# Kernel tuning notes

Hardware: AMD Instinct MI355X
Metric: run time of the kernel (lower is better)

## Reference

```python
import jax, jax.numpy as jnp
import numpy as np

D_MODEL = 1024
HIDDEN = 2048            # hidden_dimension // num_smaller_experts_per_expert
E_ROUTED = 14            # total_num_experts*num_smaller - num_shared
E_SHARED = 2
TOP_K = 2                # num_activated*num_smaller - num_shared
EPS = 1e-9               # config.epsilon
RMS_EPS = 1.1920929e-07  # torch RMSNorm default eps=None -> finfo(float32).eps


def setup_inputs() -> dict:
    key = jax.random.key(0)
    ks = jax.random.split(key, 9)
    B, T = 2, 1024
    x = jax.random.normal(ks[0], (B, T, D_MODEL), dtype=jnp.float32)
    router_w = jax.random.normal(ks[1], (D_MODEL, E_ROUTED), dtype=jnp.float32) * 0.006
    rms_w = jnp.ones((E_ROUTED, D_MODEL), dtype=jnp.float32)
    w1 = jax.random.normal(ks[2], (E_ROUTED, D_MODEL, HIDDEN), dtype=jnp.float32) * 0.02
    w2 = jax.random.normal(ks[3], (E_ROUTED, HIDDEN, D_MODEL), dtype=jnp.float32) * 0.02
    rms_w_s = jnp.ones((E_SHARED, D_MODEL), dtype=jnp.float32)
    w1_s = jax.random.normal(ks[4], (E_SHARED, D_MODEL, HIDDEN), dtype=jnp.float32) * 0.02
    w2_s = jax.random.normal(ks[5], (E_SHARED, HIDDEN, D_MODEL), dtype=jnp.float32) * 0.02
    return {"x": x, "router_w": router_w, "rms_w": rms_w, "w1": w1, "w2": w2,
            "rms_w_s": rms_w_s, "w1_s": w1_s, "w2_s": w2_s}


def _ffn(xn, rw, W1, W2):
    # RMSNorm -> Linear -> SiLU -> Linear (dropout is identity in eval)
    ms = jnp.mean(xn * xn, axis=-1, keepdims=True)
    h = (xn * jax.lax.rsqrt(ms + RMS_EPS)) * rw
    return jax.nn.silu(h @ W1) @ W2


def reference(x, router_w, rms_w, w1, w2, rms_w_s, w1_s, w2_s):
    B, T, D = x.shape
    N = B * T
    xf = x.reshape(N, D)
    # router gates + top-k sparsification + renormalization
    gates = jax.nn.softmax(xf @ router_w, axis=-1)          # [N, E]
    top_v, top_i = jax.lax.top_k(gates, TOP_K)              # [N, K]
    masked = jnp.zeros_like(gates).at[jnp.arange(N)[:, None], top_i].set(top_v)
    masked = masked / (masked.sum(axis=-1, keepdims=True) + EPS)  # [N, E]
    # routed experts: compute each expert on all tokens, combine with sparse gate weights
    # (same math as dispatch/index_add combine since masked is 0 off the top-k)
    routed = jax.vmap(lambda rw_, W1_, W2_: _ffn(xf, rw_, W1_, W2_))(rms_w, w1, w2)  # [E, N, D]
    routed_out = jnp.einsum('end,ne->nd', routed, masked)
    # shared experts: unweighted sum
    shared = jax.vmap(lambda rw_, W1_, W2_: _ffn(xf, rw_, W1_, W2_))(rms_w_s, w1_s, w2_s).sum(0)
    return (routed_out + shared).reshape(B, T, D)
```

## Files before the change

### kernel.cpp

```cpp
#include <hip/hip_runtime.h>
#include <hip/hip_bf16.h>
#include <cstdint>
#include <cstddef>

#define D_MODEL 1024
#define HIDDEN 2048
#define E_ROUTED 14
#define E_TOT 16
#define NTOK 2048
#define NASSIGN 4096
#define NROWS 8192

typedef __bf16 bf16x8 __attribute__((ext_vector_type(8)));
typedef float f32x4 __attribute__((ext_vector_type(4)));

static __device__ __forceinline__ unsigned short f2b(float f) {
  unsigned int u = __builtin_bit_cast(unsigned int, f);
  u += 0x7fffu + ((u >> 16) & 1u);
  return (unsigned short)(u >> 16);
}

#define ASYNC_COPY16(gptr, lptr)                                                        \
  __builtin_amdgcn_global_load_lds(                                                     \
      (const __attribute__((address_space(1))) unsigned int*)(gptr),                    \
      (__attribute__((address_space(3))) unsigned int*)(lptr), 16, 0, 0)

__global__ __launch_bounds__(256) void router_kernel(
    const float* __restrict__ x, const float* __restrict__ rweight,
    int* __restrict__ topi, float* __restrict__ topw,
    unsigned short* __restrict__ xhat) {
  int n = blockIdx.x, tid = threadIdx.x;
  const float4 xv = reinterpret_cast<const float4*>(x + (size_t)n * D_MODEL)[tid];
  float ss = xv.x * xv.x + xv.y * xv.y + xv.z * xv.z + xv.w * xv.w;
  float lg[E_ROUTED];
#pragma unroll
  for (int e = 0; e < E_ROUTED; ++e) lg[e] = 0.f;
  const float xa[4] = {xv.x, xv.y, xv.z, xv.w};
#pragma unroll
  for (int i = 0; i < 4; ++i) {
    const float* rw = rweight + (size_t)(tid * 4 + i) * E_ROUTED;
    float xd = xa[i];
#pragma unroll
    for (int e = 0; e < E_ROUTED; ++e) lg[e] = fmaf(xd, rw[e], lg[e]);
  }
#pragma unroll
  for (int off = 32; off > 0; off >>= 1) {
    ss += __shfl_xor(ss, off);
#pragma unroll
    for (int e = 0; e < E_ROUTED; ++e) lg[e] += __shfl_xor(lg[e], off);
  }
  __shared__ float red[4][16];
  int wid = tid >> 6, lane = tid & 63;
  if (lane == 0) {
    red[wid][0] = ss;
#pragma unroll
    for (int e = 0; e < E_ROUTED; ++e) red[wid][1 + e] = lg[e];
  }
  __syncthreads();
  __shared__ float s_scale;
  if (tid == 0) {
    float fin[15];
    for (int v = 0; v < 15; ++v) fin[v] = red[0][v] + red[1][v] + red[2][v] + red[3][v];
    s_scale = rsqrtf(fin[0] * (1.f / D_MODEL) + 1.1920929e-07f);
    float mx = fin[1];
    for (int e = 1; e < E_ROUTED; ++e) mx = fmaxf(mx, fin[1 + e]);
    float p[E_ROUTED]; float Z = 0.f;
    for (int e = 0; e < E_ROUTED; ++e) { p[e] = __expf(fin[1 + e] - mx); Z += p[e]; }
    int i0 = 0; float v0 = p[0];
    for (int e = 1; e < E_ROUTED; ++e) if (p[e] > v0) { v0 = p[e]; i0 = e; }
    int i1 = (i0 == 0) ? 1 : 0; float v1 = p[i1];
    for (int e = 0; e < E_ROUTED; ++e) if (e != i0 && p[e] > v1) { v1 = p[e]; i1 = e; }
    v0 /= Z; v1 /= Z;
    float inv = 1.f / (v0 + v1 + 1e-9f);
    topi[2 * n] = i0; topi[2 * n + 1] = i1;
    topw[2 * n] = v0 * inv; topw[2 * n + 1] = v1 * inv;
  }
  __syncthreads();
  float sc = s_scale;
  ushort4 hx;
  hx.x = f2b(xv.x * sc); hx.y = f2b(xv.y * sc);
  hx.z = f2b(xv.z * sc); hx.w = f2b(xv.w * sc);
  reinterpret_cast<ushort4*>(xhat + (size_t)n * D_MODEL)[tid] = hx;
}

__global__ __launch_bounds__(256) void count_kernel(const int* __restrict__ topi,
                                                    int* __restrict__ goff,
                                                    int* __restrict__ cursor) {
  __shared__ int cnt[E_ROUTED];
  int tid = threadIdx.x;
  if (tid < E_ROUTED) cnt[tid] = 0;
  __syncthreads();
  for (int i = tid; i < NASSIGN; i += 256) atomicAdd(&cnt[topi[i]], 1);
  __syncthreads();
  if (tid == 0) {
    int acc = 0;
    for (int e = 0; e < E_ROUTED; ++e) { goff[e] = acc; cursor[e] = acc; acc += cnt[e]; }
    goff[E_ROUTED] = acc;
  }
}

__global__ __launch_bounds__(256) void scatter_kernel(
    const int* __restrict__ topi, const float* __restrict__ topw,
    int* __restrict__ cursor, int* __restrict__ row_token,
    float* __restrict__ row_gate, int* __restrict__ token_rows) {
  int i = blockIdx.x * 256 + threadIdx.x;
  if (i >= NASSIGN) return;
  int e = topi[i];
  int pos = atomicAdd(&cursor[e], 1);
  row_token[pos] = i >> 1;
  row_gate[pos] = topw[i];
  token_rows[i] = pos;
}

template <int K, int N, bool SCALE>
__global__ __launch_bounds__(256) void convT_kernel(
    const float* __restrict__ Wr, const float* __restrict__ Ws,
    const float* __restrict__ RWr, const float* __restrict__ RWs,
    unsigned short* __restrict__ outT) {
  __shared__ float tile[64][65];
  int g = blockIdx.z;
  const float* src = (g < E_ROUTED) ? Wr + (size_t)g * K * N
                                    : Ws + (size_t)(g - E_ROUTED) * K * N;
  const float* rw = nullptr;
  if constexpr (SCALE)
    rw = (g < E_ROUTED) ? RWr + (size_t)g * K : RWs + (size_t)(g - E_ROUTED) * K;
  int k0 = blockIdx.y * 64, nn0 = blockIdx.x * 64;
  int t = threadIdx.x;
  int kk = t >> 4, nc = (t & 15) * 4;
#pragma unroll
  for (int j = 0; j < 4; ++j) {
    int k = kk + j * 16;
    float4 v = *(const float4*)(src + (size_t)(k0 + k) * N + nn0 + nc);
    float s = 1.f;
    if constexpr (SCALE) s = rw[k0 + k];
    tile[k][nc]     = v.x * s;
    tile[k][nc + 1] = v.y * s;
    tile[k][nc + 2] = v.z * s;
    tile[k][nc + 3] = v.w * s;
  }
  __syncthreads();
  int k8 = (t & 7) * 8;
#pragma unroll
  for (int p = 0; p < 2; ++p) {
    int n = (t >> 3) + p * 32;
    uint4 pk;
    pk.x = (unsigned)f2b(tile[k8 + 0][n]) | ((unsigned)f2b(tile[k8 + 1][n]) << 16);
    pk.y = (unsigned)f2b(tile[k8 + 2][n]) | ((unsigned)f2b(tile[k8 + 3][n]) << 16);
    pk.z = (unsigned)f2b(tile[k8 + 4][n]) | ((unsigned)f2b(tile[k8 + 5][n]) << 16);
    pk.w = (unsigned)f2b(tile[k8 + 6][n]) | ((unsigned)f2b(tile[k8 + 7][n]) << 16);
    *(uint4*)(outT + ((size_t)g * N + nn0 + n) * K + k0 + k8) = pk;
  }
}

template <bool G1, int KTOT, int NTOT>
__global__ __launch_bounds__(256, 3) void ffn_gemm(
    const int* __restrict__ goff, const int* __restrict__ row_token,
    const float* __restrict__ row_gate,
    const unsigned short* __restrict__ Abase,
    const unsigned short* __restrict__ Wt,
    unsigned short* __restrict__ Hout, float* __restrict__ Yout) {
  int g = blockIdx.z;
  int grpStart, cnt;
  if (g < E_ROUTED) { grpStart = goff[g]; cnt = goff[g + 1] - goff[g]; }
  else { grpStart = NASSIGN + (g - E_ROUTED) * NTOK; cnt = NTOK; }

  {
    int NX = gridDim.x, NY = gridDim.y;
    int nwg = NX * NY;
    int d = blockIdx.y * NX + blockIdx.x;
    int cpx = nwg >> 3;
    int w = (d & 7) * cpx + (d >> 3);
    int myb = w % NY;
    int nxb = w / NY;
    if (myb * 128 >= cnt) return;
    int m0 = myb * 128;
    int n0 = nxb * 128;

    __shared__ __align__(16) char smem[32 * 1024];
    char* sA = smem;
    char* sB = smem + 16 * 1024;

    int tid = threadIdx.x, lane = tid & 63, wid = tid >> 6;
    int wr = (wid >> 1) * 64, wc = (wid & 1) * 64;
    int lrow = lane >> 3;
    int swz = lrow << 4;
    int colB = ((lane & 7) << 4) ^ swz;

    const char* aSrc[4];
    const char* bSrc[4];
#pragma unroll
    for (int i = 0; i < 4; ++i) {
      int row = wid * 32 + i * 8 + lrow;
      int rIdx = m0 + row; if (rIdx >= cnt) rIdx = cnt - 1;
      int srcRow;
      if constexpr (G1) srcRow = (g < E_ROUTED) ? row_token[grpStart + rIdx] : rIdx;
      else srcRow = grpStart + rIdx;
      aSrc[i] = (const char*)(Abase + (size_t)srcRow * KTOT) + colB;
      bSrc[i] = (const char*)(Wt + ((size_t)g * NTOT + n0 + row) * KTOT) + colB;
    }

    f32x4 acc[4][4];
#pragma unroll
    for (int m = 0; m < 4; ++m)
#pragma unroll
      for (int n = 0; n < 4; ++n)
#pragma unroll
        for (int c = 0; c < 4; ++c) acc[m][n][c] = 0.f;

    for (int kt = 0; kt < KTOT / 64; ++kt) {
#pragma unroll
      for (int i = 0; i < 4; ++i) ASYNC_COPY16(aSrc[i], sA + wid * 4096 + i * 1024);
#pragma unroll
      for (int i = 0; i < 4; ++i) ASYNC_COPY16(bSrc[i], sB + wid * 4096 + i * 1024);
#pragma unroll
      for (int i = 0; i < 4; ++i) { aSrc[i] += 128; bSrc[i] += 128; }
      __syncthreads();

#pragma unroll
      for (int ks = 0; ks < 2; ++ks) {
        int kb = ks * 64 + ((lane >> 4) << 4);
        bf16x8 af[4], bfr[4];
#pragma unroll
        for (int m = 0; m < 4; ++m) {
          int r = wr + m * 16 + (lane & 15);
          af[m] = *(const bf16x8*)(sA + (r << 7) + (kb ^ ((r & 7) << 4)));
        }
#pragma unroll
        for (int n = 0; n < 4; ++n) {
          int r = wc + n * 16 + (lane & 15);
          bfr[n] = *(const bf16x8*)(sB + (r << 7) + (kb ^ ((r & 7) << 4)));
        }
#pragma unroll
        for (int m = 0; m < 4; ++m)
#pragma unroll
          for (int n = 0; n < 4; ++n)
            acc[m][n] = __builtin_amdgcn_mfma_f32_16x16x32_bf16(af[m], bfr[n], acc[m][n], 0, 0, 0);
      }
      __syncthreads();
    }

    int lr = (lane >> 4) * 4, lc = lane & 15;
#pragma unroll
    for (int m = 0; m < 4; ++m) {
      int rloc = m0 + wr + m * 16 + lr;
#pragma unroll
      for (int j = 0; j < 4; ++j) {
        if (rloc + j < cnt) {
          size_t r = (size_t)(grpStart + rloc + j);
          if constexpr (G1) {
#pragma unroll
            for (int n = 0; n < 4; ++n) {
              float v = acc[m][n][j];
              float sv = v / (1.f + __expf(-v));
              Hout[r * HIDDEN + (n0 + wc + n * 16 + lc)] = f2b(sv);
            }
          } else {
            float gate = 1.f;
            if (g < E_ROUTED) gate = row_gate[r];
#pragma unroll
            for (int n = 0; n < 4; ++n)
              Yout[r * D_MODEL + (n0 + wc + n * 16 + lc)] = acc[m][n][j] * gate;
          }
        }
      }
    }
  }
}

__global__ __launch_bounds__(256) void combine_kernel(
    const float* __restrict__ y, const int* __restrict__ token_rows,
    float* __restrict__ out) {
  int n = blockIdx.x, tid = threadIdx.x;
  int a0 = token_rows[2 * n], a1 = token_rows[2 * n + 1];
  const float4* y0 = reinterpret_cast<const float4*>(y + (size_t)a0 * D_MODEL);
  const float4* y1 = reinterpret_cast<const float4*>(y + (size_t)a1 * D_MODEL);
  const float4* s0 = reinterpret_cast<const float4*>(y + (size_t)(NASSIGN + n) * D_MODEL);
  const float4* s1 = reinterpret_cast<const float4*>(y + (size_t)(NASSIGN + NTOK + n) * D_MODEL);
  float4 a = y0[tid], b = y1[tid], c = s0[tid], d = s1[tid];
  float4 r;
  r.x = a.x + b.x + c.x + d.x;
  r.y = a.y + b.y + c.y + d.y;
  r.z = a.z + b.z + c.z + d.z;
  r.w = a.w + b.w + c.w + d.w;
  reinterpret_cast<float4*>(out + (size_t)n * D_MODEL)[tid] = r;
}

extern "C" void kernel_launch(void* const* d_in, const int* in_sizes, int n_in,
                              void* d_out, int out_size, void* d_ws, size_t ws_size,
                              hipStream_t stream) {
  const float* x        = (const float*)d_in[0];
  const float* router_w = (const float*)d_in[1];
  const float* rms_w    = (const float*)d_in[2];
  const float* w1       = (const float*)d_in[3];
  const float* w2       = (const float*)d_in[4];
  const float* rms_w_s  = (const float*)d_in[5];
  const float* w1_s    = (const float*)d_in[6];
  const float* w2_s    = (const float*)d_in[7];
  float* out = (float*)d_out;

  char* ws = (char*)d_ws;
  unsigned short* xhat = (unsigned short*)ws;
  unsigned short* h    = (unsigned short*)(ws + ((size_t)4 << 20));
  float* y             = (float*)(ws + ((size_t)36 << 20));
  unsigned short* w1t  = (unsigned short*)(ws + ((size_t)68 << 20));
  unsigned short* w2t  = (unsigned short*)(ws + ((size_t)132 << 20));
  char* meta = ws + ((size_t)196 << 20);
  int*   topi       = (int*)(meta);
  float* topw       = (float*)(meta + (16 << 10));
  int*   row_token  = (int*)(meta + (32 << 10));
  float* row_gate   = (float*)(meta + (48 << 10));
  int*   token_rows = (int*)(meta + (64 << 10));
  int*   goff       = (int*)(meta + (80 << 10));
  int*   cursor     = (int*)(meta + (80 << 10) + 256);

  router_kernel<<<NTOK, 256, 0, stream>>>(x, router_w, topi, topw, xhat);
  count_kernel<<<1, 256, 0, stream>>>(topi, goff, cursor);
  scatter_kernel<<<NASSIGN / 256, 256, 0, stream>>>(topi, topw, cursor, row_token,
                                                    row_gate, token_rows);
  convT_kernel<D_MODEL, HIDDEN, true><<<dim3(HIDDEN / 64, D_MODEL / 64, E_TOT), 256, 0, stream>>>(
      w1, w1_s, rms_w, rms_w_s, w1t);
  convT_kernel<HIDDEN, D_MODEL, false><<<dim3(D_MODEL / 64, HIDDEN / 64, E_TOT), 256, 0, stream>>>(
      w2, w2_s, nullptr, nullptr, w2t);
  ffn_gemm<true, D_MODEL, HIDDEN><<<dim3(HIDDEN / 128, 16, E_TOT), 256, 0, stream>>>(
      goff, row_token, row_gate, xhat, w1t, h, nullptr);
  ffn_gemm<false, HIDDEN, D_MODEL><<<dim3(D_MODEL / 128, 16, E_TOT), 256, 0, stream>>>(
      goff, row_token, row_gate, h, w2t, nullptr, y);
  combine_kernel<<<NTOK, 256, 0, stream>>>(y, token_rows, out);
}
```

Baseline: 244.6 us.

## Double-buffer LDS tiles with K=32 stages to overlap loads and MFMA

Moves the grouped FFN GEMM from a single 64-wide K tile per iteration to two 16 KB LDS buffers holding 32-wide K tiles. The next tile's async global-to-LDS copy is issued before computing on the current one, leaving one barrier per iteration instead of two. The aim is to hide global load latency behind MFMA work. In exchange there are twice as many iterations with half the MFMA work each, and a new XOR swizzle for 64-byte rows, which could bring back LDS bank conflicts.

```diff
diff --git a/kernel.cpp b/kernel.cpp
--- a/kernel.cpp
+++ b/kernel.cpp
@@ -164,103 +164,109 @@
   if (g < E_ROUTED) { grpStart = goff[g]; cnt = goff[g + 1] - goff[g]; }
   else { grpStart = NASSIGN + (g - E_ROUTED) * NTOK; cnt = NTOK; }
 
-  {
-    int NX = gridDim.x, NY = gridDim.y;
-    int nwg = NX * NY;
-    int d = blockIdx.y * NX + blockIdx.x;
-    int cpx = nwg >> 3;
-    int w = (d & 7) * cpx + (d >> 3);
-    int myb = w % NY;
-    int nxb = w / NY;
-    if (myb * 128 >= cnt) return;
-    int m0 = myb * 128;
-    int n0 = nxb * 128;
-
-    __shared__ __align__(16) char smem[32 * 1024];
-    char* sA = smem;
-    char* sB = smem + 16 * 1024;
-
-    int tid = threadIdx.x, lane = tid & 63, wid = tid >> 6;
-    int wr = (wid >> 1) * 64, wc = (wid & 1) * 64;
-    int lrow = lane >> 3;
-    int swz = lrow << 4;
-    int colB = ((lane & 7) << 4) ^ swz;
-
-    const char* aSrc[4];
-    const char* bSrc[4];
-#pragma unroll
-    for (int i = 0; i < 4; ++i) {
-      int row = wid * 32 + i * 8 + lrow;
-      int rIdx = m0 + row; if (rIdx >= cnt) rIdx = cnt - 1;
-      int srcRow;
-      if constexpr (G1) srcRow = (g < E_ROUTED) ? row_token[grpStart + rIdx] : rIdx;
-      else srcRow = grpStart + rIdx;
-      aSrc[i] = (const char*)(Abase + (size_t)srcRow * KTOT) + colB;
-      bSrc[i] = (const char*)(Wt + ((size_t)g * NTOT + n0 + row) * KTOT) + colB;
+  int NX = gridDim.x, NY = gridDim.y;
+  int nwg = NX * NY;
+  int d = blockIdx.y * NX + blockIdx.x;
+  int cpx = nwg >> 3;
+  int w = (d & 7) * cpx + (d >> 3);
+  int myb = w % NY;
+  int nxb = w / NY;
+  if (myb * 128 >= cnt) return;
+  int m0 = myb * 128;
+  int n0 = nxb * 128;
+
+  __shared__ __align__(16) char smem[2][16 * 1024];
+
+  int tid = threadIdx.x, lane = tid & 63, wid = tid >> 6;
+  int wr = (wid >> 1) * 64, wc = (wid & 1) * 64;
+
+  int lrow4 = lane >> 2;
+  int gsrc = ((lane & 3) ^ (lrow4 & 3)) * 16;
+  const char* aSrc[2];
+  const char* bSrc[2];
+#pragma unroll
+  for (int i = 0; i < 2; ++i) {
+    int row = wid * 32 + i * 16 + lrow4;
+    int rIdx = m0 + row; if (rIdx >= cnt) rIdx = cnt - 1;
+    int srcRow;
+    if constexpr (G1) srcRow = (g < E_ROUTED) ? row_token[grpStart + rIdx] : rIdx;
+    else srcRow = grpStart + rIdx;
+    aSrc[i] = (const char*)(Abase + (size_t)srcRow * KTOT) + gsrc;
+    bSrc[i] = (const char*)(Wt + ((size_t)g * NTOT + n0 + row) * KTOT) + gsrc;
+  }
+
+  f32x4 acc[4][4];
+#pragma unroll
+  for (int m = 0; m < 4; ++m)
+#pragma unroll
+    for (int n = 0; n < 4; ++n)
+#pragma unroll
+      for (int c = 0; c < 4; ++c) acc[m][n][c] = 0.f;
+
+  auto STAGE = [&](int buf) {
+    char* sA = smem[buf];
+    char* sB = smem[buf] + 8192;
+#pragma unroll
+    for (int i = 0; i < 2; ++i) ASYNC_COPY16(aSrc[i], sA + wid * 2048 + i * 1024);
+#pragma unroll
+    for (int i = 0; i < 2; ++i) ASYNC_COPY16(bSrc[i], sB + wid * 2048 + i * 1024);
+#pragma unroll
+    for (int i = 0; i < 2; ++i) { aSrc[i] += 64; bSrc[i] += 64; }
+  };
+
+  int l15 = lane & 15;
+  int qx = ((lane >> 4) ^ (l15 & 3)) * 16;
+  auto COMPUTE = [&](int buf) {
+    const char* sA = smem[buf];
+    const char* sB = smem[buf] + 8192;
+    bf16x8 af[4], bfr[4];
+#pragma unroll
+    for (int m = 0; m < 4; ++m) {
+      int r = wr + m * 16 + l15;
+      af[m] = *(const bf16x8*)(sA + (r << 6) + qx);
     }
-
-    f32x4 acc[4][4];
+#pragma unroll
+    for (int n = 0; n < 4; ++n) {
+      int r = wc + n * 16 + l15;
+      bfr[n] = *(const bf16x8*)(sB + (r << 6) + qx);
+    }
 #pragma unroll
     for (int m = 0; m < 4; ++m)
 #pragma unroll
       for (int n = 0; n < 4; ++n)
-#pragma unroll
-        for (int c = 0; c < 4; ++c) acc[m][n][c] = 0.f;
-
-    for (int kt = 0; kt < KTOT / 64; ++kt) {
-#pragma unroll
-      for (int i = 0; i < 4; ++i) ASYNC_COPY16(aSrc[i], sA + wid * 4096 + i * 1024);
-#pragma unroll
-      for (int i = 0; i < 4; ++i) ASYNC_COPY16(bSrc[i], sB + wid * 4096 + i * 1024);
-#pragma unroll
-      for (int i = 0; i < 4; ++i) { aSrc[i] += 128; bSrc[i] += 128; }
-      __syncthreads();
-
-#pragma unroll
-      for (int ks = 0; ks < 2; ++ks) {
-        int kb = ks * 64 + ((lane >> 4) << 4);
-        bf16x8 af[4], bfr[4];
-#pragma unroll
-        for (int m = 0; m < 4; ++m) {
-          int r = wr + m * 16 + (lane & 15);
-          af[m] = *(const bf16x8*)(sA + (r << 7) + (kb ^ ((r & 7) << 4)));
-        }
-#pragma unroll
-        for (int n = 0; n < 4; ++n) {
-          int r = wc + n * 16 + (lane & 15);
-          bfr[n] = *(const bf16x8*)(sB + (r << 7) + (kb ^ ((r & 7) << 4)));
-        }
-#pragma unroll
-        for (int m = 0; m < 4; ++m)
+        acc[m][n] = __builtin_amdgcn_mfma_f32_16x16x32_bf16(af[m], bfr[n], acc[m][n], 0, 0, 0);
+  };
+
+  constexpr int NT = KTOT / 32;
+  STAGE(0);
+  __syncthreads();
+  for (int kt = 0; kt < NT; ++kt) {
+    if (kt + 1 < NT) STAGE((kt + 1) & 1);
+    COMPUTE(kt & 1);
+    __syncthreads();
+  }
+
+  int lr = (lane >> 4) * 4, lc = lane & 15;
+#pragma unroll
+  for (int m = 0; m < 4; ++m) {
+    int rloc = m0 + wr + m * 16 + lr;
+#pragma unroll
+    for (int j = 0; j < 4; ++j) {
+      if (rloc + j < cnt) {
+        size_t r = (size_t)(grpStart + rloc + j);
+        if constexpr (G1) {
+#pragma unroll
+          for (int n = 0; n < 4; ++n) {
+            float v = acc[m][n][j];
+            float sv = v / (1.f + __expf(-v));
+            Hout[r * HIDDEN + (n0 + wc + n * 16 + lc)] = f2b(sv);
+          }
+        } else {
+          float gate = 1.f;
+          if (g < E_ROUTED) gate = row_gate[r];
 #pragma unroll
           for (int n = 0; n < 4; ++n)
-            acc[m][n] = __builtin_amdgcn_mfma_f32_16x16x32_bf16(af[m], bfr[n], acc[m][n], 0, 0, 0);
-      }
-      __syncthreads();
-    }
-
-    int lr = (lane >> 4) * 4, lc = lane & 15;
-#pragma unroll
-    for (int m = 0; m < 4; ++m) {
-      int rloc = m0 + wr + m * 16 + lr;
-#pragma unroll
-      for (int j = 0; j < 4; ++j) {
-        if (rloc + j < cnt) {
-          size_t r = (size_t)(grpStart + rloc + j);
-          if constexpr (G1) {
-#pragma unroll
-            for (int n = 0; n < 4; ++n) {
-              float v = acc[m][n][j];
-              float sv = v / (1.f + __expf(-v));
-              Hout[r * HIDDEN + (n0 + wc + n * 16 + lc)] = f2b(sv);
-            }
-          } else {
-            float gate = 1.f;
-            if (g < E_ROUTED) gate = row_gate[r];
-#pragma unroll
-            for (int n = 0; n < 4; ++n)
-              Yout[r * D_MODEL + (n0 + wc + n * 16 + lc)] = acc[m][n][j] * gate;
-          }
+            Yout[r * D_MODEL + (n0 + wc + n * 16 + lc)] = acc[m][n][j] * gate;
         }
       }
     }
```

After: 255.8 us. 1.05x slower.
